# Kernel tuning notes

Hardware: AMD Instinct MI355X
Metric: run time of the kernel (lower is better)

## Reference

```python
import jax, jax.numpy as jnp
import numpy as np
import math

N_TOTAL = 262144
C = 128
B = 512
LMAX = 512  # max segment length (static for jit)


def setup_inputs() -> dict:
    key = jax.random.key(0)
    ks = jax.random.split(key, 8)
    Q_feature = jax.random.normal(ks[0], (N_TOTAL, C), dtype=jnp.float32)
    K_feature = jax.random.normal(ks[1], (N_TOTAL, C), dtype=jnp.float32)
    # cumulative offsets: equal segments of length LMAX (general code handles ragged)
    offset = (jnp.arange(1, B + 1, dtype=jnp.int64) * (N_TOTAL // B))
    s = 1.0 / math.sqrt(C)
    Wq = jax.random.normal(ks[2], (C, C), dtype=jnp.float32) * s
    Wk = jax.random.normal(ks[3], (C, C), dtype=jnp.float32) * s
    Wv = jax.random.normal(ks[4], (C, C), dtype=jnp.float32) * s
    bq = jnp.zeros((C,), dtype=jnp.float32)
    bk = jnp.zeros((C,), dtype=jnp.float32)
    bv = jnp.zeros((C,), dtype=jnp.float32)
    return {"Q_feature": Q_feature, "K_feature": K_feature,
            "Wq": Wq, "bq": bq, "Wk": Wk, "bk": bk, "Wv": Wv, "bv": bv,
            "offset": offset}


def reference(Q_feature, K_feature, Wq, bq, Wk, bk, Wv, bv, offset):
    N, Cdim = Q_feature.shape
    Q = Q_feature @ Wq.T + bq
    K = K_feature @ Wk.T + bk
    V = K_feature @ Wv.T + bv

    starts = jnp.concatenate([jnp.zeros((1,), offset.dtype), offset[:-1]])
    lengths = offset - starts                         # (B,)
    pos = jnp.arange(LMAX)                            # (LMAX,)
    idx = jnp.clip(starts[:, None] + pos[None, :], 0, N - 1)  # (B, LMAX)
    mask = pos[None, :] < lengths[:, None]            # (B, LMAX) valid tokens

    Qp = Q[idx]                                       # (B, LMAX, C)
    Kp = K[idx]
    Vp = V[idx]

    scale = 1.0 / math.sqrt(Cdim)
    scores = jnp.einsum('blc,bmc->blm', Qp, Kp) * scale     # (B, LMAX, LMAX)
    scores = jnp.where(mask[:, None, :], scores, jnp.float32(-1e30))
    attn = jax.nn.softmax(scores, axis=-1)
    outp = jnp.einsum('blm,bmc->blc', attn, Vp)             # (B, LMAX, C)
    outp = outp * mask[:, :, None]                          # zero padded rows

    # scatter padded segments back to flat (N, C); idx is an exact partition on valid rows
    out = jnp.zeros((N, Cdim), dtype=outp.dtype).at[idx].add(outp)
    return out
```

## Files before the change

### kernel.cpp

```cpp
#include <hip/hip_runtime.h>
#include <hip/hip_bf16.h>

#define CDIM 128
#define LMAXC 512
#define QBLK 128
#define KVBLK 64

#define QSCALE (0.08838834764831845f * 1.4426950408889634f)

typedef __attribute__((ext_vector_type(8))) short bf16x8;
typedef __attribute__((ext_vector_type(4))) short bf16x4;
typedef __attribute__((ext_vector_type(4))) float f32x4;

__device__ inline short f2bf(float f) {
    union { float f; unsigned u; } v; v.f = f;
    unsigned r = v.u + 0x7FFFu + ((v.u >> 16) & 1u);
    return (short)(r >> 16);
}

__device__ inline bf16x8 cvt8v(float4 a, float4 b) {
    bf16x8 o;
    o[0] = f2bf(a.x); o[1] = f2bf(a.y); o[2] = f2bf(a.z); o[3] = f2bf(a.w);
    o[4] = f2bf(b.x); o[5] = f2bf(b.y); o[6] = f2bf(b.z); o[7] = f2bf(b.w);
    return o;
}

__device__ inline unsigned pk2(float lo, float hi) {
    unsigned r;
    asm("v_cvt_pk_bf16_f32 %0, %1, %2" : "=v"(r) : "v"(lo), "v"(hi));
    return r;
}

__device__ inline void gload16(const void* g, void* l) {
    __builtin_amdgcn_global_load_lds(
        (const __attribute__((address_space(1))) unsigned*)g,
        (__attribute__((address_space(3))) unsigned*)l, 16, 0, 0);
}

__device__ inline void blk_barrier() {
    __builtin_amdgcn_sched_barrier(0);
    __builtin_amdgcn_s_barrier();
    __builtin_amdgcn_sched_barrier(0);
}

__device__ inline int pch(int q) { return ((q + (q >> 3)) & 7) << 4; }

__global__ void wcvt_kernel(const float* __restrict__ Wq,
                            const float* __restrict__ Wk,
                            const float* __restrict__ Wv,
                            short* __restrict__ Wbf)
{
    int t = blockIdx.x * 256 + threadIdx.x;
    int m = t / 2048;
    int e = (t % 2048) * 8;
    const float* W = (m == 0) ? Wq : (m == 1) ? Wk : Wv;
    float sc = (m == 0) ? QSCALE : 1.0f;
    float4 a = *reinterpret_cast<const float4*>(W + e);
    float4 b = *reinterpret_cast<const float4*>(W + e + 4);
    a.x *= sc; a.y *= sc; a.z *= sc; a.w *= sc;
    b.x *= sc; b.y *= sc; b.z *= sc; b.w *= sc;
    *reinterpret_cast<bf16x8*>(Wbf + m * 16384 + e) = cvt8v(a, b);
}

__device__ inline void tile_qk(const char* __restrict__ wlds,
                               const bf16x8 xfr[2][4],
                               const float* __restrict__ bias, float bsc,
                               short* __restrict__ outp, int rowb,
                               int lrow, int lhalf)
{
#pragma unroll
    for (int cf = 0; cf < 8; ++cf) {
        const int key = cf * 16 + lrow;
        bf16x8 wfr[4];
#pragma unroll
        for (int ks = 0; ks < 4; ++ks) {
            int wb = (key * 256 + (ks * 32 + lhalf * 8) * 2) ^ ((key & 7) << 4);
            wfr[ks] = *reinterpret_cast<const bf16x8*>(wlds + wb);
        }
        float4 bv4 = *reinterpret_cast<const float4*>(bias + cf * 16 + lhalf * 4);
#pragma unroll
        for (int xt = 0; xt < 2; ++xt) {
            f32x4 acc = {0.f, 0.f, 0.f, 0.f};
#pragma unroll
            for (int ks = 0; ks < 4; ++ks)
                acc = __builtin_amdgcn_mfma_f32_16x16x32_bf16(wfr[ks], xfr[xt][ks], acc, 0, 0, 0);
            bf16x4 pk;
            pk[0] = f2bf(acc[0] + bv4.x * bsc);
            pk[1] = f2bf(acc[1] + bv4.y * bsc);
            pk[2] = f2bf(acc[2] + bv4.z * bsc);
            pk[3] = f2bf(acc[3] + bv4.w * bsc);
            *reinterpret_cast<bf16x4*>(
                outp + (size_t)(rowb + xt * 16 + lrow) * CDIM
                     + cf * 16 + lhalf * 4) = pk;
        }
    }
}

__device__ inline void tile_v(const char* __restrict__ wlds,
                              const bf16x8 xfr[2][4],
                              const float* __restrict__ bv,
                              short* __restrict__ Vt, int rowb, int N,
                              int lrow, int lhalf)
{
#pragma unroll
    for (int cf = 0; cf < 8; ++cf) {
        const int d = cf * 16 + lrow;
        bf16x8 wfr[4];
#pragma unroll
        for (int ks = 0; ks < 4; ++ks) {
            int wb = (d * 256 + (ks * 32 + lhalf * 8) * 2) ^ ((d & 7) << 4);
            wfr[ks] = *reinterpret_cast<const bf16x8*>(wlds + wb);
        }
        f32x4 acc0 = {0.f, 0.f, 0.f, 0.f};
        f32x4 acc1 = {0.f, 0.f, 0.f, 0.f};
#pragma unroll
        for (int ks = 0; ks < 4; ++ks) {
            acc0 = __builtin_amdgcn_mfma_f32_16x16x32_bf16(xfr[0][ks], wfr[ks], acc0, 0, 0, 0);
            acc1 = __builtin_amdgcn_mfma_f32_16x16x32_bf16(xfr[1][ks], wfr[ks], acc1, 0, 0, 0);
        }
        float bcol = bv[d];
        bf16x4 p0, p1;
#pragma unroll
        for (int r = 0; r < 4; ++r) {
            p0[r] = f2bf(acc0[r] + bcol);
            p1[r] = f2bf(acc1[r] + bcol);
        }
        short* vrow = Vt + (size_t)d * N + rowb + lhalf * 4;
        *reinterpret_cast<bf16x4*>(vrow)      = p0;
        *reinterpret_cast<bf16x4*>(vrow + 16) = p1;
    }
}

__global__ __launch_bounds__(512) void projkv_kernel(
    const float* __restrict__ Kf, const short* __restrict__ Wbf,
    const float* __restrict__ bk, const float* __restrict__ bv,
    short* __restrict__ Kp, short* __restrict__ Vt, int N)
{
    __shared__ __align__(16) char wlds[32768];

    const int tid   = threadIdx.x;
    const int lane  = tid & 63;
    const int wv    = tid >> 6;
    const int lrow  = lane & 15;
    const int lhalf = lane >> 4;
    const int rowb  = blockIdx.x * 256 + wv * 32;

#pragma unroll
    for (int j = 0; j < 4; ++j) {
        int beta = j * 8192 + tid * 16;
        int r  = beta >> 8;
        int gs = ((beta >> 4) & 15) ^ (r & 7);
        gload16(Wbf + 16384 + r * 128 + gs * 8, wlds + beta);
    }

    bf16x8 xfr[2][4];
#pragma unroll
    for (int xt = 0; xt < 2; ++xt) {
        const float* xr = Kf + (size_t)(rowb + xt * 16 + lrow) * CDIM + lhalf * 8;
#pragma unroll
        for (int ks = 0; ks < 4; ++ks) {
            const float4* s = reinterpret_cast<const float4*>(xr + ks * 32);
            xfr[xt][ks] = cvt8v(s[0], s[1]);
        }
    }
    __syncthreads();

    tile_qk(wlds, xfr, bk, 1.0f, Kp, rowb, lrow, lhalf);
    __syncthreads();
#pragma unroll
    for (int j = 0; j < 4; ++j) {
        int beta = j * 8192 + tid * 16;
        int r  = beta >> 8;
        int gs = ((beta >> 4) & 15) ^ (r & 7);
        gload16(Wbf + 32768 + r * 128 + gs * 8, wlds + beta);
    }
    __syncthreads();
    tile_v(wlds, xfr, bv, Vt, rowb, N, lrow, lhalf);
}

__global__ __launch_bounds__(256) void attn_kernel(
    const float* __restrict__ Qf, const short* __restrict__ Wbf,
    const float* __restrict__ bq,
    const short* __restrict__ Kp, const short* __restrict__ VtG,
    const int* __restrict__ offset, float* __restrict__ out, int Ntot)
{
    __shared__ __align__(16) char smem[81920];
    char* lds_p = smem + 65536;

    const int nq = LMAXC / QBLK;
    int flat = blockIdx.x, total = gridDim.x;
    int seg, qb;
    if ((total & (8 * nq - 1)) == 0) {
        int per = total >> 3;
        int xcd = flat & 7;
        int wi  = flat >> 3;
        int sl  = wi / nq;
        qb  = wi - sl * nq;
        seg = xcd * (per / nq) + sl;
    } else { seg = flat / nq; qb = flat - seg * nq; }

    const int start = (seg == 0) ? 0 : offset[seg - 1];
    int len = offset[seg] - start;
    if (len > LMAXC) len = LMAXC;
    const int q0 = qb * QBLK;
    if (q0 >= len) return;

    const int tid   = threadIdx.x;
    const int lane  = tid & 63;
    const int wv    = tid >> 6;
    const int lrow  = lane & 15;
    const int lhalf = lane >> 4;
    const int ntiles = (len + KVBLK - 1) / KVBLK;
    const int lm1 = len - 1;

    bf16x8 aq[2][4];
    {
        char* qstage = smem + 32768 + wv * 8192;

        bf16x8 xq[2][4];
#pragma unroll
        for (int qt = 0; qt < 2; ++qt) {
            int qr = q0 + wv * 32 + qt * 16 + lrow;
            if (qr > lm1) qr = lm1;
            const float* xr = Qf + (size_t)(start + qr) * CDIM + lhalf * 8;
#pragma unroll
            for (int ks = 0; ks < 4; ++ks) {
                const float4* s = reinterpret_cast<const float4*>(xr + ks * 32);
                xq[qt][ks] = cvt8v(s[0], s[1]);
            }
        }
#pragma unroll
        for (int cf = 0; cf < 8; ++cf) {
            const int key = cf * 16 + lrow;
            bf16x8 wfr[4];
#pragma unroll
            for (int ks = 0; ks < 4; ++ks)
                wfr[ks] = *reinterpret_cast<const bf16x8*>(
                    Wbf + key * CDIM + ks * 32 + lhalf * 8);
            float4 bq4 = *reinterpret_cast<const float4*>(bq + cf * 16 + lhalf * 4);
#pragma unroll
            for (int qt = 0; qt < 2; ++qt) {
                f32x4 acc = {0.f, 0.f, 0.f, 0.f};
#pragma unroll
                for (int ks = 0; ks < 4; ++ks)
                    acc = __builtin_amdgcn_mfma_f32_16x16x32_bf16(wfr[ks], xq[qt][ks], acc, 0, 0, 0);
                bf16x4 pk;
                pk[0] = f2bf(acc[0] + bq4.x * QSCALE);
                pk[1] = f2bf(acc[1] + bq4.y * QSCALE);
                pk[2] = f2bf(acc[2] + bq4.z * QSCALE);
                pk[3] = f2bf(acc[3] + bq4.w * QSCALE);
                int ql = qt * 16 + lrow;
                *reinterpret_cast<bf16x4*>(
                    qstage + ql * 256 + ((cf * 32 + lhalf * 8) ^ pch(ql))) = pk;
            }
        }
        asm volatile("s_waitcnt lgkmcnt(0)" ::: "memory");
#pragma unroll
        for (int qt = 0; qt < 2; ++qt) {
            int ql = qt * 16 + lrow;
#pragma unroll
            for (int ks = 0; ks < 4; ++ks)
                aq[qt][ks] = *reinterpret_cast<const bf16x8*>(
                    qstage + ql * 256 + ((ks * 64 + lhalf * 16) ^ pch(ql)));
        }
    }
    __syncthreads();

    auto stage = [&](int kv0, int bb) {
        char* kb = smem + bb * 32768;
        char* vb = kb + 16384;
#pragma unroll
        for (int j = 0; j < 4; ++j) {
            int beta = j * 4096 + wv * 1024 + (lane << 4);
            int r  = beta >> 8;
            int gs = ((beta >> 4) & 15) ^ (r & 7);
            int rg = kv0 + r; if (rg > lm1) rg = lm1;
            gload16(Kp + (((size_t)(start + rg)) << 7) + (gs << 3),
                    kb + j * 4096 + wv * 1024);
            int d   = beta >> 7;
            int gs2 = ((beta >> 4) & 7) ^ (d & 7);
            long gk = (long)start + kv0 + (gs2 << 3);
            if (gk + 8 > Ntot) gk = Ntot - 8;
            gload16(VtG + (size_t)d * Ntot + gk,
                    vb + j * 4096 + wv * 1024);
        }
    };

    stage(0, 0);

    f32x4 acc_o[2][8];
    float lsum[2] = {0.f, 0.f};
#pragma unroll
    for (int qt = 0; qt < 2; ++qt)
#pragma unroll
        for (int df = 0; df < 8; ++df) acc_o[qt][df] = (f32x4){0.f, 0.f, 0.f, 0.f};

    const int wbase = wv * 4096;

    for (int t = 0; t < ntiles; ++t) {
        const int kv0 = t * KVBLK;
        const int bb  = t & 1;
        if (t + 1 < ntiles) {
            stage(kv0 + KVBLK, bb ^ 1);
            asm volatile("s_waitcnt vmcnt(8)" ::: "memory");
        } else {
            asm volatile("s_waitcnt vmcnt(0)" ::: "memory");
        }
        blk_barrier();

        char* lds_k  = smem + bb * 32768;
        char* lds_vt = lds_k + 16384;
        const bool tail = (kv0 + KVBLK > len);

        f32x4 s0[4], s1[4];
        __builtin_amdgcn_s_setprio(1);
#pragma unroll
        for (int kf = 0; kf < 4; ++kf) {
            s0[kf] = (f32x4){0.f, 0.f, 0.f, 0.f};
            s1[kf] = (f32x4){0.f, 0.f, 0.f, 0.f};
            int key = kf * 16 + lrow;
#pragma unroll
            for (int ks = 0; ks < 4; ++ks) {
                int kbo = (key * 256 + (ks * 32 + lhalf * 8) * 2) ^ ((key & 7) << 4);
                bf16x8 kfr = *reinterpret_cast<const bf16x8*>(lds_k + kbo);
                s0[kf] = __builtin_amdgcn_mfma_f32_16x16x32_bf16(kfr, aq[0][ks], s0[kf], 0, 0, 0);
                s1[kf] = __builtin_amdgcn_mfma_f32_16x16x32_bf16(kfr, aq[1][ks], s1[kf], 0, 0, 0);
            }
        }
        __builtin_amdgcn_s_setprio(0);

        const int keyb0 = kv0 + lhalf * 4;
#pragma unroll
        for (int qt = 0; qt < 2; ++qt) {
            const int qlocal = qt * 16 + lrow;
            const int rowoff = wbase + qlocal * 128;
            const int swz = pch(qlocal);
#pragma unroll
            for (int kf = 0; kf < 4; ++kf) {
                f32x4 sv = qt ? s1[kf] : s0[kf];
                float p[4];
#pragma unroll
                for (int r = 0; r < 4; ++r) {
                    float pv = exp2f(sv[r]);
                    if (tail && (keyb0 + kf * 16 + r >= len)) pv = 0.f;
                    p[r] = pv;
                    lsum[qt] += pv;
                }
                unsigned long long w =
                    (unsigned long long)pk2(p[0], p[1]) |
                    ((unsigned long long)pk2(p[2], p[3]) << 32);
                *reinterpret_cast<unsigned long long*>(
                    lds_p + rowoff + ((kf * 32 + lhalf * 8) ^ swz)) = w;
            }
        }

        __builtin_amdgcn_s_setprio(1);
#pragma unroll
        for (int ks2 = 0; ks2 < 2; ++ks2) {
            bf16x8 ap0 = *reinterpret_cast<const bf16x8*>(
                lds_p + wbase + lrow * 128 + ((ks2 * 64 + lhalf * 16) ^ pch(lrow)));
            bf16x8 ap1 = *reinterpret_cast<const bf16x8*>(
                lds_p + wbase + (16 + lrow) * 128 + ((ks2 * 64 + lhalf * 16) ^ pch(16 + lrow)));
            int k0 = ks2 * 32 + lhalf * 8;
#pragma unroll
            for (int df = 0; df < 8; ++df) {
                int d = df * 16 + lrow;
                int vb2 = (d * 128 + k0 * 2) ^ ((d & 7) << 4);
                bf16x8 bvf = *reinterpret_cast<const bf16x8*>(lds_vt + vb2);
                acc_o[0][df] = __builtin_amdgcn_mfma_f32_16x16x32_bf16(ap0, bvf, acc_o[0][df], 0, 0, 0);
                acc_o[1][df] = __builtin_amdgcn_mfma_f32_16x16x32_bf16(ap1, bvf, acc_o[1][df], 0, 0, 0);
            }
        }
        __builtin_amdgcn_s_setprio(0);

        blk_barrier();
    }

#pragma unroll
    for (int qt = 0; qt < 2; ++qt) {
        float l = lsum[qt];
        l += __shfl_xor(l, 16);
        l += __shfl_xor(l, 32);
        float rinv[4];
#pragma unroll
        for (int r = 0; r < 4; ++r)
            rinv[r] = 1.0f / __shfl(l, lhalf * 4 + r);
#pragma unroll
        for (int df = 0; df < 8; ++df)
#pragma unroll
            for (int r = 0; r < 4; ++r) {
                int qg = q0 + wv * 32 + qt * 16 + lhalf * 4 + r;
                if (qg < len)
                    out[(size_t)(start + qg) * CDIM + df * 16 + lrow]
                        = acc_o[qt][df][r] * rinv[r];
            }
    }
}

extern "C" void kernel_launch(void* const* d_in, const int* in_sizes, int n_in,
                              void* d_out, int out_size, void* d_ws, size_t ws_size,
                              hipStream_t stream) {
    const float* Qf = (const float*)d_in[0];
    const float* Kf = (const float*)d_in[1];
    const float* Wq = (const float*)d_in[2];
    const float* bq = (const float*)d_in[3];
    const float* Wk = (const float*)d_in[4];
    const float* bk = (const float*)d_in[5];
    const float* Wv = (const float*)d_in[6];
    const float* bv_ = (const float*)d_in[7];
    const int* offset = (const int*)d_in[8];

    const int N = in_sizes[0] / CDIM;
    const int B = in_sizes[8];

    short* Wbf = (short*)d_ws;
    short* Kp  = Wbf + 3 * 16384;
    short* Vt  = Kp + (size_t)N * CDIM;
    float* out = (float*)d_out;

    wcvt_kernel<<<24, 256, 0, stream>>>(Wq, Wk, Wv, Wbf);

    projkv_kernel<<<dim3(N / 256), 512, 0, stream>>>(Kf, Wbf, bk, bv_,
                                                     Kp, Vt, N);

    attn_kernel<<<dim3(B * (LMAXC / QBLK)), 256, 0, stream>>>(
        Qf, Wbf, bq, Kp, Vt, offset, out, N);
}
```

Baseline: 234.6 us.

## Split Q projection out of attention kernel into separate projection pass

Moves the Q projection (fp32 load, bf16 convert, MFMA against Wq, bias and scale) out of the attention kernel into a new projq_kernel that writes bf16 Q to workspace. The attention kernel then loads precomputed bf16 Q fragments straight from global memory after issuing the first K/V stage, which drops the LDS staging and the per-block weight loads. The cost is an extra kernel launch and a round trip of N*C bf16 through global memory, traded against a shorter attention prologue with lower register and LDS pressure.

```diff
diff --git a/kernel.cpp b/kernel.cpp
--- a/kernel.cpp
+++ b/kernel.cpp
@@ -131,10 +131,9 @@
     }
 }
 
-__global__ __launch_bounds__(512) void projkv_kernel(
-    const float* __restrict__ Kf, const short* __restrict__ Wbf,
-    const float* __restrict__ bk, const float* __restrict__ bv,
-    short* __restrict__ Kp, short* __restrict__ Vt, int N)
+__global__ __launch_bounds__(512) void projq_kernel(
+    const float* __restrict__ Qf, const short* __restrict__ Wbf,
+    const float* __restrict__ bq, short* __restrict__ Qp)
 {
     __shared__ __align__(16) char wlds[32768];
 
@@ -150,6 +149,43 @@
         int beta = j * 8192 + tid * 16;
         int r  = beta >> 8;
         int gs = ((beta >> 4) & 15) ^ (r & 7);
+        gload16(Wbf + r * 128 + gs * 8, wlds + beta);
+    }
+
+    bf16x8 xfr[2][4];
+#pragma unroll
+    for (int xt = 0; xt < 2; ++xt) {
+        const float* xr = Qf + (size_t)(rowb + xt * 16 + lrow) * CDIM + lhalf * 8;
+#pragma unroll
+        for (int ks = 0; ks < 4; ++ks) {
+            const float4* s = reinterpret_cast<const float4*>(xr + ks * 32);
+            xfr[xt][ks] = cvt8v(s[0], s[1]);
+        }
+    }
+    __syncthreads();
+
+    tile_qk(wlds, xfr, bq, QSCALE, Qp, rowb, lrow, lhalf);
+}
+
+__global__ __launch_bounds__(512) void projkv_kernel(
+    const float* __restrict__ Kf, const short* __restrict__ Wbf,
+    const float* __restrict__ bk, const float* __restrict__ bv,
+    short* __restrict__ Kp, short* __restrict__ Vt, int N)
+{
+    __shared__ __align__(16) char wlds[32768];
+
+    const int tid   = threadIdx.x;
+    const int lane  = tid & 63;
+    const int wv    = tid >> 6;
+    const int lrow  = lane & 15;
+    const int lhalf = lane >> 4;
+    const int rowb  = blockIdx.x * 256 + wv * 32;
+
+#pragma unroll
+    for (int j = 0; j < 4; ++j) {
+        int beta = j * 8192 + tid * 16;
+        int r  = beta >> 8;
+        int gs = ((beta >> 4) & 15) ^ (r & 7);
         gload16(Wbf + 16384 + r * 128 + gs * 8, wlds + beta);
     }
 
@@ -179,10 +215,9 @@
 }
 
 __global__ __launch_bounds__(256) void attn_kernel(
-    const float* __restrict__ Qf, const short* __restrict__ Wbf,
-    const float* __restrict__ bq,
-    const short* __restrict__ Kp, const short* __restrict__ VtG,
-    const int* __restrict__ offset, float* __restrict__ out, int Ntot)
+    const short* __restrict__ Qp, const short* __restrict__ Kp,
+    const short* __restrict__ VtG, const int* __restrict__ offset,
+    float* __restrict__ out, int Ntot)
 {
     __shared__ __align__(16) char smem[81920];
     char* lds_p = smem + 65536;
@@ -212,59 +247,6 @@
     const int lhalf = lane >> 4;
     const int ntiles = (len + KVBLK - 1) / KVBLK;
     const int lm1 = len - 1;
-
-    bf16x8 aq[2][4];
-    {
-        char* qstage = smem + 32768 + wv * 8192;
-
-        bf16x8 xq[2][4];
-#pragma unroll
-        for (int qt = 0; qt < 2; ++qt) {
-            int qr = q0 + wv * 32 + qt * 16 + lrow;
-            if (qr > lm1) qr = lm1;
-            const float* xr = Qf + (size_t)(start + qr) * CDIM + lhalf * 8;
-#pragma unroll
-            for (int ks = 0; ks < 4; ++ks) {
-                const float4* s = reinterpret_cast<const float4*>(xr + ks * 32);
-                xq[qt][ks] = cvt8v(s[0], s[1]);
-            }
-        }
-#pragma unroll
-        for (int cf = 0; cf < 8; ++cf) {
-            const int key = cf * 16 + lrow;
-            bf16x8 wfr[4];
-#pragma unroll
-            for (int ks = 0; ks < 4; ++ks)
-                wfr[ks] = *reinterpret_cast<const bf16x8*>(
-                    Wbf + key * CDIM + ks * 32 + lhalf * 8);
-            float4 bq4 = *reinterpret_cast<const float4*>(bq + cf * 16 + lhalf * 4);
-#pragma unroll
-            for (int qt = 0; qt < 2; ++qt) {
-                f32x4 acc = {0.f, 0.f, 0.f, 0.f};
-#pragma unroll
-                for (int ks = 0; ks < 4; ++ks)
-                    acc = __builtin_amdgcn_mfma_f32_16x16x32_bf16(wfr[ks], xq[qt][ks], acc, 0, 0, 0);
-                bf16x4 pk;
-                pk[0] = f2bf(acc[0] + bq4.x * QSCALE);
-                pk[1] = f2bf(acc[1] + bq4.y * QSCALE);
-                pk[2] = f2bf(acc[2] + bq4.z * QSCALE);
-                pk[3] = f2bf(acc[3] + bq4.w * QSCALE);
-                int ql = qt * 16 + lrow;
-                *reinterpret_cast<bf16x4*>(
-                    qstage + ql * 256 + ((cf * 32 + lhalf * 8) ^ pch(ql))) = pk;
-            }
-        }
-        asm volatile("s_waitcnt lgkmcnt(0)" ::: "memory");
-#pragma unroll
-        for (int qt = 0; qt < 2; ++qt) {
-            int ql = qt * 16 + lrow;
-#pragma unroll
-            for (int ks = 0; ks < 4; ++ks)
-                aq[qt][ks] = *reinterpret_cast<const bf16x8*>(
-                    qstage + ql * 256 + ((ks * 64 + lhalf * 16) ^ pch(ql)));
-        }
-    }
-    __syncthreads();
 
     auto stage = [&](int kv0, int bb) {
         char* kb = smem + bb * 32768;
@@ -288,6 +270,17 @@
 
     stage(0, 0);
 
+    bf16x8 aq[2][4];
+#pragma unroll
+    for (int qt = 0; qt < 2; ++qt) {
+        int qr = q0 + wv * 32 + qt * 16 + lrow;
+        if (qr > lm1) qr = lm1;
+        const short* qrow = Qp + (size_t)(start + qr) * CDIM;
+#pragma unroll
+        for (int ks = 0; ks < 4; ++ks)
+            aq[qt][ks] = *reinterpret_cast<const bf16x8*>(qrow + ks * 32 + lhalf * 8);
+    }
+
     f32x4 acc_o[2][8];
     float lsum[2] = {0.f, 0.f};
 #pragma unroll
@@ -414,15 +407,18 @@
     const int B = in_sizes[8];
 
     short* Wbf = (short*)d_ws;
-    short* Kp  = Wbf + 3 * 16384;
+    short* Qp  = Wbf + 3 * 16384;
+    short* Kp  = Qp + (size_t)N * CDIM;
     short* Vt  = Kp + (size_t)N * CDIM;
     float* out = (float*)d_out;
 
     wcvt_kernel<<<24, 256, 0, stream>>>(Wq, Wk, Wv, Wbf);
 
+    projq_kernel<<<dim3(N / 256), 512, 0, stream>>>(Qf, Wbf, bq, Qp);
+
     projkv_kernel<<<dim3(N / 256), 512, 0, stream>>>(Kf, Wbf, bk, bv_,
                                                      Kp, Vt, N);
 
     attn_kernel<<<dim3(B * (LMAXC / QBLK)), 256, 0, stream>>>(
-        Qf, Wbf, bq, Kp, Vt, offset, out, N);
-}
+        Qp, Kp, Vt, offset, out, N);
+}
```

Result: slower. 262.3 us (+11.8%).
